# Kernel tuning notes

Hardware: AMD Instinct MI355X
Metric: run time of the kernel (lower is better)

Reference implementation:

```python
import jax, jax.numpy as jnp
import numpy as np

B, S, D = 8, 2048, 512
DK = 64  # attention_dim

def setup_inputs() -> dict:
    key = jax.random.key(0)
    k0, k1, k2, k3 = jax.random.split(key, 4)
    inputs = jax.random.normal(k0, (B, S, D), dtype=jnp.float32)
    # add_weight initializer='random_normal' -> stddev 0.05 in keras
    W_q = jax.random.normal(k1, (D, DK), dtype=jnp.float32) * 0.05
    W_k = jax.random.normal(k2, (D, DK), dtype=jnp.float32) * 0.05
    W_v = jax.random.normal(k3, (D, DK), dtype=jnp.float32) * 0.05
    return {"inputs": inputs, "W_q": W_q, "W_k": W_k, "W_v": W_v}

def reference(inputs, W_q, W_k, W_v):
    # QKV projections: [B,S,D] @ [D,DK] -> [B,S,DK]
    q = jnp.einsum('bsd,dk->bsk', inputs, W_q)
    k = jnp.einsum('bsd,dk->bsk', inputs, W_k)
    v = jnp.einsum('bsd,dk->bsk', inputs, W_v)
    scale = 1.0 / jnp.sqrt(jnp.asarray(DK, dtype=q.dtype))
    scores = jnp.einsum('bqk,bsk->bqs', q, k) * scale  # [B,S,S]
    weights = jax.nn.softmax(scores, axis=-1)
    attended = jnp.einsum('bqs,bsk->bqk', weights, v)  # [B,S,DK]
    return attended, weights
```

## Files before the change

kernel.cpp:

```cpp
#include <hip/hip_runtime.h>


typedef __bf16 bf16x8 __attribute__((ext_vector_type(8)));
typedef float f32x4 __attribute__((ext_vector_type(4)));

__device__ __forceinline__ short f2bf(float f) {
    unsigned u = __builtin_bit_cast(unsigned, f);
    u = (u + 0x7fffu + ((u >> 16) & 1u)) >> 16;
    return (short)u;
}
__device__ __forceinline__ float bf2f(short h) {
    unsigned u = ((unsigned)(unsigned short)h) << 16;
    return __builtin_bit_cast(float, u);
}
__device__ __forceinline__ bf16x8 ldfrag(const short* p) {
    return *reinterpret_cast<const bf16x8*>(p);
}
__device__ __forceinline__ f32x4 mfma16(bf16x8 a, bf16x8 b, f32x4 c) {
    return __builtin_amdgcn_mfma_f32_16x16x32_bf16(a, b, c, 0, 0, 0);
}

__global__ void wtrans_kernel(const float* __restrict__ Wq,
                              const float* __restrict__ Wk,
                              const float* __restrict__ Wv,
                              short* __restrict__ wt_hi,
                              short* __restrict__ wt_lo) {
    int idx = blockIdx.x * 256 + threadIdx.x;
    int k = idx & 511;
    int n = (idx >> 9) & 63;
    int m = idx >> 15;
    const float* W = (m == 0) ? Wq : (m == 1) ? Wk : Wv;
    float w = W[k * 64 + n];
    short hi = f2bf(w);
    wt_hi[idx] = hi;
    if (m < 2) wt_lo[idx] = f2bf(w - bf2f(hi));
}

__global__ __launch_bounds__(256) void qkv_kernel(
    const float* __restrict__ x,
    const short* __restrict__ wt_hi, const short* __restrict__ wt_lo,
    short* __restrict__ Qg, short* __restrict__ Kg, short* __restrict__ VTg) {
  __shared__ __align__(16) short Ah[32 * 40], Al[32 * 40];
  __shared__ __align__(16) short Bqh[64 * 40], Bql[64 * 40];
  __shared__ __align__(16) short Bkh[64 * 40], Bkl[64 * 40];
  __shared__ __align__(16) short Bvh[64 * 40];
  const int t = threadIdx.x;
  const int wave = t >> 6, lane = t & 63, quad = lane >> 4, l15 = lane & 15;
  const int rg = wave & 1, ntp = wave >> 1;
  const int rbase = blockIdx.x * 32;

  f32x4 accq[2] = {}, acck[2] = {}, accv[2] = {};

  for (int k0 = 0; k0 < 512; k0 += 32) {
    {
      int row = t >> 3, off = (t & 7) << 2;
      float4 v = *(const float4*)(x + (size_t)(rbase + row) * 512 + k0 + off);
      short4 h, lo;
      h.x = f2bf(v.x); lo.x = f2bf(v.x - bf2f(h.x));
      h.y = f2bf(v.y); lo.y = f2bf(v.y - bf2f(h.y));
      h.z = f2bf(v.z); lo.z = f2bf(v.z - bf2f(h.z));
      h.w = f2bf(v.w); lo.w = f2bf(v.w - bf2f(h.w));
      *(short4*)(Ah + row * 40 + off) = h;
      *(short4*)(Al + row * 40 + off) = lo;
    }
    {
      int row = t >> 2, off = (t & 3) << 3;
      int src = row * 512 + k0 + off;
      int dst = row * 40 + off;
      *(int4*)(Bqh + dst) = *(const int4*)(wt_hi + 0 * 32768 + src);
      *(int4*)(Bkh + dst) = *(const int4*)(wt_hi + 1 * 32768 + src);
      *(int4*)(Bvh + dst) = *(const int4*)(wt_hi + 2 * 32768 + src);
      *(int4*)(Bql + dst) = *(const int4*)(wt_lo + 0 * 32768 + src);
      *(int4*)(Bkl + dst) = *(const int4*)(wt_lo + 1 * 32768 + src);
    }
    __syncthreads();
    bf16x8 ah = ldfrag(Ah + (rg * 16 + l15) * 40 + quad * 8);
    bf16x8 al = ldfrag(Al + (rg * 16 + l15) * 40 + quad * 8);
    #pragma unroll
    for (int j = 0; j < 2; j++) {
      const int nt = ntp * 2 + j;
      const int boff = (nt * 16 + l15) * 40 + quad * 8;
      bf16x8 bh = ldfrag(Bqh + boff);
      accq[j] = mfma16(ah, bh, accq[j]);
      accq[j] = mfma16(al, bh, accq[j]);
      accq[j] = mfma16(ah, ldfrag(Bql + boff), accq[j]);
      bh = ldfrag(Bkh + boff);
      acck[j] = mfma16(ah, bh, acck[j]);
      acck[j] = mfma16(al, bh, acck[j]);
      acck[j] = mfma16(ah, ldfrag(Bkl + boff), acck[j]);
      accv[j] = mfma16(ah, ldfrag(Bvh + boff), accv[j]);
    }
    __syncthreads();
  }
  #pragma unroll
  for (int j = 0; j < 2; j++) {
    const int nt = ntp * 2 + j;
    #pragma unroll
    for (int r = 0; r < 4; r++) {
      int row = rbase + rg * 16 + quad * 4 + r;
      int col = nt * 16 + l15;
      Qg[(size_t)row * 64 + col] = f2bf(accq[j][r]);
      Kg[(size_t)row * 64 + col] = f2bf(acck[j][r]);
    }
  }
  short* vt = Ah;
  #pragma unroll
  for (int j = 0; j < 2; j++) {
    const int col = (ntp * 2 + j) * 16 + l15;
    short4 p;
    p.x = f2bf(accv[j][0]); p.y = f2bf(accv[j][1]);
    p.z = f2bf(accv[j][2]); p.w = f2bf(accv[j][3]);
    *(short4*)(vt + col * 40 + rg * 16 + quad * 4) = p;
  }
  __syncthreads();
  {
    const int bidx = rbase >> 11;
    int c = t >> 2, ch = (t & 3) << 3;
    *(int4*)(VTg + (size_t)bidx * 131072 + (size_t)c * 2048 + (rbase & 2047) + ch) =
        *(const int4*)(vt + c * 40 + ch);
  }
}

__global__ __launch_bounds__(256) void lpass_kernel(
    const short* __restrict__ Qg, const short* __restrict__ Kg,
    float* __restrict__ Lpart) {
  __shared__ __align__(16) short Ks[128 * 72];
  __shared__ float Lb[4][16];
  const int t = threadIdx.x;
  const int wave = t >> 6, lane = t & 63, quad = lane >> 4, l15 = lane & 15;
  const int rg = wave & 1, half = wave >> 1;
  const int b = blockIdx.x, qbase = blockIdx.y * 32, sc = blockIdx.z;
  const float sc2 = 0.125f * 1.44269504088896340736f;
  const float C0 = 16.0f;

  const short* Kb = Kg + (size_t)b * 131072;
  const short* qp =
      Qg + (size_t)(b * 2048 + qbase + rg * 16 + l15) * 64 + quad * 8;
  const bf16x8 aq0 = ldfrag(qp);
  const bf16x8 aq1 = ldfrag(qp + 32);

  float lsum = 0.f;
  for (int s0 = 0; s0 < 512; s0 += 128) {
    const int sg = sc * 512 + s0;
    #pragma unroll
    for (int i = 0; i < 4; i++) {
      int c = t + i * 256, row = c >> 3, off = (c & 7) << 3;
      *(int4*)(Ks + row * 72 + off) =
          *(const int4*)(Kb + (size_t)(sg + row) * 64 + off);
    }
    __syncthreads();
    #pragma unroll
    for (int nt2 = 0; nt2 < 4; nt2++) {
      const int koff = ((half * 4 + nt2) * 16 + l15) * 72 + quad * 8;
      f32x4 c = {};
      c = mfma16(ldfrag(Ks + koff), aq0, c);
      c = mfma16(ldfrag(Ks + koff + 32), aq1, c);
      #pragma unroll
      for (int r = 0; r < 4; r++) lsum += exp2f(c[r] * sc2 - C0);
    }
    __syncthreads();
  }
  lsum += __shfl_xor(lsum, 16);
  lsum += __shfl_xor(lsum, 32);
  if (lane < 16) Lb[wave][lane] = lsum;
  __syncthreads();
  if (half == 0 && lane < 16)
    Lpart[(size_t)sc * 16384 + b * 2048 + qbase + rg * 16 + lane] =
        Lb[wave][lane] + Lb[wave ^ 2][lane];
}

__global__ __launch_bounds__(256) void wo_kernel(
    const short* __restrict__ Qg, const short* __restrict__ Kg,
    const short* __restrict__ VTg, const float* __restrict__ Lpart,
    float* __restrict__ w_out, float* __restrict__ Opart) {
  __shared__ __align__(16) short Ks[64 * 72];
  __shared__ __align__(16) short Vs[64 * 72];
  __shared__ __align__(16) short Plds[4 * 16 * 72];
  const int t = threadIdx.x;
  const int wave = t >> 6, lane = t & 63, quad = lane >> 4, l15 = lane & 15;
  const int b = blockIdx.x, qbase = blockIdx.y * 64, sc = blockIdx.z;
  const float sc2 = 0.125f * 1.44269504088896340736f;
  const float C0 = 16.0f;

  const short* Kb = Kg + (size_t)b * 131072;
  const short* Vb = VTg + (size_t)b * 131072;
  const int qrow = b * 2048 + qbase + wave * 16 + l15;
  const short* qp = Qg + (size_t)qrow * 64 + quad * 8;
  const bf16x8 aq0 = ldfrag(qp);
  const bf16x8 aq1 = ldfrag(qp + 32);
  const float invl = 1.0f / (Lpart[qrow] + Lpart[16384 + qrow] +
                             Lpart[32768 + qrow] + Lpart[49152 + qrow]);

  f32x4 acc[4] = {};
  float* wrow = w_out + (size_t)qrow * 2048 + sc * 512;
  short* pl = Plds + wave * (16 * 72) + l15 * 72;

  for (int s0 = 0; s0 < 512; s0 += 64) {
    const int sg = sc * 512 + s0;
    #pragma unroll
    for (int i = 0; i < 2; i++) {
      int c = t + i * 256, row = c >> 3, off = (c & 7) << 3;
      *(int4*)(Ks + row * 72 + off) =
          *(const int4*)(Kb + (size_t)(sg + row) * 64 + off);
      *(int4*)(Vs + row * 72 + off) =
          *(const int4*)(Vb + (size_t)row * 2048 + sg + off);
    }
    __syncthreads();
    #pragma unroll
    for (int nt2 = 0; nt2 < 4; nt2++) {
      const int koff = (nt2 * 16 + l15) * 72 + quad * 8;
      f32x4 c = {};
      c = mfma16(ldfrag(Ks + koff), aq0, c);
      c = mfma16(ldfrag(Ks + koff + 32), aq1, c);
      f32x4 w;
      #pragma unroll
      for (int r = 0; r < 4; r++) w[r] = exp2f(c[r] * sc2 - C0) * invl;
      *(f32x4*)(wrow + s0 + nt2 * 16 + quad * 4) = w;
      short4 pb;
      pb.x = f2bf(w[0]); pb.y = f2bf(w[1]);
      pb.z = f2bf(w[2]); pb.w = f2bf(w[3]);
      *(short4*)(pl + nt2 * 16 + quad * 4) = pb;
    }
    asm volatile("s_waitcnt lgkmcnt(0)" ::: "memory");
    #pragma unroll
    for (int ks2 = 0; ks2 < 2; ks2++) {
      bf16x8 ap = ldfrag(pl + ks2 * 32 + quad * 8);
      #pragma unroll
      for (int nc = 0; nc < 4; nc++)
        acc[nc] = mfma16(
            ap, ldfrag(Vs + (nc * 16 + l15) * 72 + ks2 * 32 + quad * 8),
            acc[nc]);
    }
    __syncthreads();
  }
  #pragma unroll
  for (int nc = 0; nc < 4; nc++)
    #pragma unroll
    for (int r = 0; r < 4; r++)
      Opart[((size_t)sc * 16384 + b * 2048 + qbase + wave * 16 + quad * 4 + r) *
                64 + nc * 16 + l15] = acc[nc][r];
}

__global__ __launch_bounds__(256) void finalize_kernel(
    const float* __restrict__ Opart, float* __restrict__ att_out) {
  int idx = blockIdx.x * 256 + threadIdx.x;
  int row = idx >> 4, c4 = (idx & 15) << 2;
  size_t base = (size_t)row * 64 + c4;
  f32x4 o = *(const f32x4*)(Opart + base);
  o += *(const f32x4*)(Opart + 1048576 + base);
  o += *(const f32x4*)(Opart + 2097152 + base);
  o += *(const f32x4*)(Opart + 3145728 + base);
  *(f32x4*)(att_out + base) = o;
}

extern "C" void kernel_launch(void* const* d_in, const int* in_sizes, int n_in,
                              void* d_out, int out_size, void* d_ws, size_t ws_size,
                              hipStream_t stream) {
  const float* x  = (const float*)d_in[0];
  const float* Wq = (const float*)d_in[1];
  const float* Wk = (const float*)d_in[2];
  const float* Wv = (const float*)d_in[3];

  char* ws = (char*)d_ws;
  short* wt_hi = (short*)(ws + 0);
  short* wt_lo = (short*)(ws + 196608);
  short* Qg    = (short*)(ws + 327680);
  short* Kg    = (short*)(ws + 327680 + 2097152);
  short* VTg   = (short*)(ws + 327680 + 4194304);
  float* Lpart = (float*)(ws + 6619136);
  float* Opart = (float*)(ws + 6881280);

  float* att  = (float*)d_out;
  float* wout = att + (size_t)8 * 2048 * 64;

  hipLaunchKernelGGL(wtrans_kernel, dim3(384), dim3(256), 0, stream,
                     Wq, Wk, Wv, wt_hi, wt_lo);
  hipLaunchKernelGGL(qkv_kernel, dim3(512), dim3(256), 0, stream,
                     x, wt_hi, wt_lo, Qg, Kg, VTg);
  hipLaunchKernelGGL(lpass_kernel, dim3(8, 64, 4), dim3(256), 0, stream,
                     Qg, Kg, Lpart);
  hipLaunchKernelGGL(wo_kernel, dim3(8, 32, 4), dim3(256), 0, stream,
                     Qg, Kg, VTg, Lpart, wout, Opart);
  hipLaunchKernelGGL(finalize_kernel, dim3(1024), dim3(256), 0, stream,
                     Opart, att);
}
```

Before: 219.8 us.

## Widen lpass to 64 query rows per block and store partial outputs in bf16

The row-sum pass now gives each wave its own 16 query rows across all 128 keys of a tile. This halves the grid, so each K tile loaded into LDS serves twice as many queries, and the LDS cross-wave reduction with its extra barrier goes away. The split-K partial attention outputs are stored as bf16 instead of fp32, halving Opart write and read traffic. The finalize kernel is changed to match, with each thread handling 8 columns. Rounding partial outputs to bf16 adds precision loss to the attended output.

```diff
diff --git a/kernel.cpp b/kernel.cpp
--- a/kernel.cpp
+++ b/kernel.cpp
@@ -3,6 +3,7 @@
 
 typedef __bf16 bf16x8 __attribute__((ext_vector_type(8)));
 typedef float f32x4 __attribute__((ext_vector_type(4)));
+typedef short short8_t __attribute__((ext_vector_type(8)));
 
 __device__ __forceinline__ short f2bf(float f) {
     unsigned u = __builtin_bit_cast(unsigned, f);
@@ -125,17 +126,15 @@
     const short* __restrict__ Qg, const short* __restrict__ Kg,
     float* __restrict__ Lpart) {
   __shared__ __align__(16) short Ks[128 * 72];
-  __shared__ float Lb[4][16];
   const int t = threadIdx.x;
   const int wave = t >> 6, lane = t & 63, quad = lane >> 4, l15 = lane & 15;
-  const int rg = wave & 1, half = wave >> 1;
-  const int b = blockIdx.x, qbase = blockIdx.y * 32, sc = blockIdx.z;
+  const int b = blockIdx.x, qbase = blockIdx.y * 64, sc = blockIdx.z;
   const float sc2 = 0.125f * 1.44269504088896340736f;
   const float C0 = 16.0f;
 
   const short* Kb = Kg + (size_t)b * 131072;
-  const short* qp =
-      Qg + (size_t)(b * 2048 + qbase + rg * 16 + l15) * 64 + quad * 8;
+  const int qrow = b * 2048 + qbase + wave * 16 + l15;
+  const short* qp = Qg + (size_t)qrow * 64 + quad * 8;
   const bf16x8 aq0 = ldfrag(qp);
   const bf16x8 aq1 = ldfrag(qp + 32);
 
@@ -150,8 +149,8 @@
     }
     __syncthreads();
     #pragma unroll
-    for (int nt2 = 0; nt2 < 4; nt2++) {
-      const int koff = ((half * 4 + nt2) * 16 + l15) * 72 + quad * 8;
+    for (int nt = 0; nt < 8; nt++) {
+      const int koff = (nt * 16 + l15) * 72 + quad * 8;
       f32x4 c = {};
       c = mfma16(ldfrag(Ks + koff), aq0, c);
       c = mfma16(ldfrag(Ks + koff + 32), aq1, c);
@@ -162,17 +161,14 @@
   }
   lsum += __shfl_xor(lsum, 16);
   lsum += __shfl_xor(lsum, 32);
-  if (lane < 16) Lb[wave][lane] = lsum;
-  __syncthreads();
-  if (half == 0 && lane < 16)
-    Lpart[(size_t)sc * 16384 + b * 2048 + qbase + rg * 16 + lane] =
-        Lb[wave][lane] + Lb[wave ^ 2][lane];
+  if (lane < 16)
+    Lpart[(size_t)sc * 16384 + b * 2048 + qbase + wave * 16 + lane] = lsum;
 }
 
 __global__ __launch_bounds__(256) void wo_kernel(
     const short* __restrict__ Qg, const short* __restrict__ Kg,
     const short* __restrict__ VTg, const float* __restrict__ Lpart,
-    float* __restrict__ w_out, float* __restrict__ Opart) {
+    float* __restrict__ w_out, short* __restrict__ Opart) {
   __shared__ __align__(16) short Ks[64 * 72];
   __shared__ __align__(16) short Vs[64 * 72];
   __shared__ __align__(16) short Plds[4 * 16 * 72];
@@ -238,19 +234,27 @@
     #pragma unroll
     for (int r = 0; r < 4; r++)
       Opart[((size_t)sc * 16384 + b * 2048 + qbase + wave * 16 + quad * 4 + r) *
-                64 + nc * 16 + l15] = acc[nc][r];
+                64 + nc * 16 + l15] = f2bf(acc[nc][r]);
 }
 
 __global__ __launch_bounds__(256) void finalize_kernel(
-    const float* __restrict__ Opart, float* __restrict__ att_out) {
+    const short* __restrict__ Opart, float* __restrict__ att_out) {
   int idx = blockIdx.x * 256 + threadIdx.x;
-  int row = idx >> 4, c4 = (idx & 15) << 2;
-  size_t base = (size_t)row * 64 + c4;
-  f32x4 o = *(const f32x4*)(Opart + base);
-  o += *(const f32x4*)(Opart + 1048576 + base);
-  o += *(const f32x4*)(Opart + 2097152 + base);
-  o += *(const f32x4*)(Opart + 3145728 + base);
-  *(f32x4*)(att_out + base) = o;
+  int row = idx >> 3, c8 = (idx & 7) << 3;
+  size_t base = (size_t)row * 64 + c8;
+  short8_t p0 = *(const short8_t*)(Opart + base);
+  short8_t p1 = *(const short8_t*)(Opart + 1048576 + base);
+  short8_t p2 = *(const short8_t*)(Opart + 2097152 + base);
+  short8_t p3 = *(const short8_t*)(Opart + 3145728 + base);
+  f32x4 oA, oB;
+  #pragma unroll
+  for (int j = 0; j < 4; j++) {
+    oA[j] = (bf2f(p0[j]) + bf2f(p1[j])) + (bf2f(p2[j]) + bf2f(p3[j]));
+    oB[j] = (bf2f(p0[4 + j]) + bf2f(p1[4 + j])) +
+            (bf2f(p2[4 + j]) + bf2f(p3[4 + j]));
+  }
+  *(f32x4*)(att_out + base) = oA;
+  *(f32x4*)(att_out + base + 4) = oB;
 }
 
 extern "C" void kernel_launch(void* const* d_in, const int* in_sizes, int n_in,
@@ -268,7 +272,7 @@
   short* Kg    = (short*)(ws + 327680 + 2097152);
   short* VTg   = (short*)(ws + 327680 + 4194304);
   float* Lpart = (float*)(ws + 6619136);
-  float* Opart = (float*)(ws + 6881280);
+  short* Opart = (short*)(ws + 6881280);
 
   float* att  = (float*)d_out;
   float* wout = att + (size_t)8 * 2048 * 64;
@@ -277,10 +281,10 @@
                      Wq, Wk, Wv, wt_hi, wt_lo);
   hipLaunchKernelGGL(qkv_kernel, dim3(512), dim3(256), 0, stream,
                      x, wt_hi, wt_lo, Qg, Kg, VTg);
-  hipLaunchKernelGGL(lpass_kernel, dim3(8, 64, 4), dim3(256), 0, stream,
+  hipLaunchKernelGGL(lpass_kernel, dim3(8, 32, 4), dim3(256), 0, stream,
                      Qg, Kg, Lpart);
   hipLaunchKernelGGL(wo_kernel, dim3(8, 32, 4), dim3(256), 0, stream,
                      Qg, Kg, VTg, Lpart, wout, Opart);
-  hipLaunchKernelGGL(finalize_kernel, dim3(1024), dim3(256), 0, stream,
+  hipLaunchKernelGGL(finalize_kernel, dim3(512), dim3(256), 0, stream,
                      Opart, att);
 }
```

After: 215.8 us. Within noise of the previous version (-1.8%).
